# Kernel optimization log

Measured on AMD Instinct MI355X. Metric: run time of the kernel, lower is better.

## Reference

```python
import jax, jax.numpy as jnp
import numpy as np

EXPERT_NUM = 64
EXPERT_USE = 8
AUX_LOSS_LAMBDA = 0.01


def setup_inputs() -> dict:
    key = jax.random.key(0)
    k1, k2 = jax.random.split(key)
    h = jax.random.normal(k1, (4, 4096, 2048), dtype=jnp.float32)
    # nn.Linear(embed_dim, expert_num) weight: [expert_num, embed_dim], ~U(-1/sqrt(d), 1/sqrt(d))
    bound = 1.0 / np.sqrt(2048.0)
    W = jax.random.uniform(k2, (EXPERT_NUM, 2048), dtype=jnp.float32,
                           minval=-bound, maxval=bound)
    return {"h": h, "W": W}


def reference(h, W):
    b, s, d = h.shape
    hf = h.reshape(-1, d)                              # [b*s, d]
    logits = jnp.einsum('nd,ed->ne', hf, W)            # [b*s, E]
    scores = jax.nn.softmax(logits, axis=-1)           # [b*s, E]
    expert_scores, expert_ids = jax.lax.top_k(scores, EXPERT_USE)  # [b*s, k]
    expert_weight = expert_scores / jnp.sum(expert_scores, axis=-1, keepdims=True)
    # L2 load-balance aux loss (training mode, lambda > 0)
    seq_probs = scores.reshape(b, s, EXPERT_NUM).mean(axis=1)      # [b, E]
    aux_loss = jnp.mean(jnp.sum(seq_probs ** 2, axis=-1)) * EXPERT_NUM * AUX_LOSS_LAMBDA
    return expert_ids, expert_weight, aux_loss
```

## Files before the change

### kernel.cpp

```cpp
#include <hip/hip_runtime.h>
#include <math.h>

#define NTOK 16384
#define DIM 2048
#define NEXP 64
#define TOPK 8
#define BT 64
#define KC 32
#define NCHUNK (DIM / KC)
#define PADK 36
#define NBLK (NTOK / BT)
#define EPW 4

typedef float f2 __attribute__((ext_vector_type(2)));
typedef float f4 __attribute__((ext_vector_type(4)));

__device__ __forceinline__ f2 pk_mul(f2 a, f2 b) {
    f2 d; asm("v_pk_mul_f32 %0, %1, %2" : "=v"(d) : "v"(a), "v"(b)); return d;
}
__device__ __forceinline__ f2 pk_add(f2 a, f2 b) {
    f2 d; asm("v_pk_add_f32 %0, %1, %2" : "=v"(d) : "v"(a), "v"(b)); return d;
}

__global__ __launch_bounds__(1024, 1) void moe_gate_np(
    const float* __restrict__ h, const float* __restrict__ W,
    float* __restrict__ out, float* __restrict__ wsum)
{
#pragma clang fp contract(off)
    __shared__ float sA[2][BT * PADK];
    __shared__ float sB[2][NEXP * PADK];
    __shared__ float lg[BT][NEXP + 2];

    const int tid  = threadIdx.x;
    const int lane = tid & 63;
    const int wv   = tid >> 6;
    const int blk  = blockIdx.x;
    const long tok0 = (long)blk * BT;
    const float* hA = h + tok0 * DIM;
    const int e0 = wv * EPW;

    const int sidx = tid & 511;
    const int srow = sidx >> 3;
    const int scol = (sidx & 7) * 4;
    const bool isA = tid < 512;
    const float* gsrc = isA ? (hA + (long)srow * DIM + scol)
                            : (W  + (long)srow * DIM + scol);
    float* l0 = isA ? &sA[0][srow * PADK + scol] : &sB[0][srow * PADK + scol];
    float* l1 = isA ? &sA[1][srow * PADK + scol] : &sB[1][srow * PADK + scol];

    f4 pa = *(const f4*)gsrc;
    *(f4*)l0 = pa;
    pa = *(const f4*)(gsrc + KC);

    f2 a01[EPW], a23[EPW];
    #pragma unroll
    for (int j = 0; j < EPW; ++j) { a01[j] = (f2)(0.f); a23[j] = (f2)(0.f); }

    for (int kc = 0; kc < NCHUNK; ++kc) {
        __syncthreads();
        const int cur = kc & 1;

        if (kc + 1 < NCHUNK)
            *(f4*)(cur ? l0 : l1) = pa;
        if (kc + 2 < NCHUNK)
            pa = *(const f4*)(gsrc + (long)(kc + 2) * KC);

        #pragma unroll
        for (int s = 0; s < 2; ++s) {
            f4 af[4];
            const float* ab = &sA[cur][lane * PADK + s * 16];
            #pragma unroll
            for (int v = 0; v < 4; ++v) af[v] = *(const f4*)(ab + 4 * v);

            f2 alo[4], ahi[4];
            #pragma unroll
            for (int v = 0; v < 4; ++v) {
                alo[v] = __builtin_shufflevector(af[v], af[v], 0, 1);
                ahi[v] = __builtin_shufflevector(af[v], af[v], 2, 3);
            }

            const float* bb = &sB[cur][e0 * PADK + s * 16];
            #pragma unroll
            for (int j = 0; j < EPW; ++j) {
                f4 Bf[4];
                #pragma unroll
                for (int v = 0; v < 4; ++v)
                    Bf[v] = *(const f4*)(bb + j * PADK + 4 * v);

                f2 blo[4], bhi[4];
                #pragma unroll
                for (int v = 0; v < 4; ++v) {
                    blo[v] = __builtin_shufflevector(Bf[v], Bf[v], 0, 1);
                    bhi[v] = __builtin_shufflevector(Bf[v], Bf[v], 2, 3);
                }
                f2 x;
                x = pk_add(pk_mul(blo[3], alo[3]), a01[j]);
                x = pk_add(pk_mul(blo[2], alo[2]), x);
                x = pk_add(pk_mul(blo[1], alo[1]), x);
                a01[j] = pk_add(pk_mul(blo[0], alo[0]), x);
                x = pk_add(pk_mul(bhi[3], ahi[3]), a23[j]);
                x = pk_add(pk_mul(bhi[2], ahi[2]), x);
                x = pk_add(pk_mul(bhi[1], ahi[1]), x);
                a23[j] = pk_add(pk_mul(bhi[0], ahi[0]), x);
            }
        }
    }

    #pragma unroll
    for (int j = 0; j < EPW; ++j) {
        f2 s2 = pk_add(a01[j], a23[j]);
        lg[lane][e0 + j] = s2.x + s2.y;
    }
    __syncthreads();

    float auxacc = 0.f;

    for (int tt = 0; tt < 4; ++tt) {
        const int t = wv * 4 + tt;
        const float s = lg[t][lane];

        float m = s;
        #pragma unroll
        for (int off = 32; off >= 1; off >>= 1)
            m = fmaxf(m, __shfl_xor(m, off));

        const float p = expf(s - m);
        lg[t][lane] = p;
        __asm__ volatile("" ::: "memory");

        float r0s = lg[t][0], r1s = lg[t][1], r2s = lg[t][2], r3s = lg[t][3];
        float r4s = lg[t][4], r5s = lg[t][5], r6s = lg[t][6], r7s = lg[t][7];
        #pragma unroll
        for (int i = 1; i < 8; ++i) {
            r0s += lg[t][8 * i + 0]; r1s += lg[t][8 * i + 1];
            r2s += lg[t][8 * i + 2]; r3s += lg[t][8 * i + 3];
            r4s += lg[t][8 * i + 4]; r5s += lg[t][8 * i + 5];
            r6s += lg[t][8 * i + 6]; r7s += lg[t][8 * i + 7];
        }
        const float S = ((r0s + r1s) + (r2s + r3s)) + ((r4s + r5s) + (r6s + r7s));

        const float score = p / S;
        auxacc += score;

        float cv = score;
        float myv = 0.f;
        int   myi = 0;
        #pragma unroll
        for (int i = 0; i < TOPK; ++i) {
            float v = cv;
            int idx = lane;
            #pragma unroll
            for (int off = 32; off >= 1; off >>= 1) {
                float v2 = __shfl_xor(v, off);
                int   i2 = __shfl_xor(idx, off);
                if (v2 > v || (v2 == v && i2 < idx)) { v = v2; idx = i2; }
            }
            if (lane == i)   { myv = v; myi = idx; }
            if (lane == idx) cv = -1.f;
        }

        float S8 = 0.f;
        #pragma unroll
        for (int r = 0; r < TOPK; ++r) S8 += __shfl(myv, r);

        if (lane < TOPK) {
            const long o = (tok0 + t) * TOPK + lane;
            out[o]                     = (float)myi;
            out[(long)NTOK * TOPK + o] = myv / S8;
        }
    }

    const int b = blk >> 6;
    atomicAdd(&wsum[b * NEXP + lane], auxacc);
}

__global__ void aux_finish(const float* __restrict__ wsum, float* __restrict__ out)
{
    const int lane = threadIdx.x;
    float a = 0.f;
    #pragma unroll
    for (int b = 0; b < 4; ++b) {
        const float v = wsum[b * NEXP + lane] * (1.0f / 4096.0f);
        a = fmaf(v, v, a);
    }
    #pragma unroll
    for (int off = 32; off >= 1; off >>= 1)
        a += __shfl_xor(a, off);
    if (lane == 0)
        out[2L * NTOK * TOPK] = a * 0.25f * (float)NEXP * 0.01f;
}

extern "C" void kernel_launch(void* const* d_in, const int* in_sizes, int n_in,
                              void* d_out, int out_size, void* d_ws, size_t ws_size,
                              hipStream_t stream) {
    const float* h = (const float*)d_in[0];
    const float* W = (const float*)d_in[1];
    float* out  = (float*)d_out;
    float* wsum = (float*)d_ws;

    hipMemsetAsync(d_ws, 0, 1024, stream);
    moe_gate_np<<<NBLK, 1024, 0, stream>>>(h, W, out, wsum);
    aux_finish<<<1, 64, 0, stream>>>(wsum, out);
}
```

Measured before the change: 153.8 us.

## Load half of each wave's gate weights via scalar loads instead of LDS

```diff
diff --git a/kernel.cpp b/kernel.cpp
--- a/kernel.cpp
+++ b/kernel.cpp
@@ -12,9 +12,13 @@
 #define NBLK (NTOK / BT)
 #define EPW 4
 
-typedef float f2 __attribute__((ext_vector_type(2)));
-typedef float f4 __attribute__((ext_vector_type(4)));
-
+typedef float f2  __attribute__((ext_vector_type(2)));
+typedef float f4  __attribute__((ext_vector_type(4)));
+typedef float f16 __attribute__((ext_vector_type(16)));
+
+__device__ __forceinline__ f2 pk_mul_sv(f2 bs, f2 av) {
+    f2 d; asm("v_pk_mul_f32 %0, %1, %2" : "=v"(d) : "s"(bs), "v"(av)); return d;
+}
 __device__ __forceinline__ f2 pk_mul(f2 a, f2 b) {
     f2 d; asm("v_pk_mul_f32 %0, %1, %2" : "=v"(d) : "v"(a), "v"(b)); return d;
 }
@@ -28,7 +32,7 @@
 {
 #pragma clang fp contract(off)
     __shared__ float sA[2][BT * PADK];
-    __shared__ float sB[2][NEXP * PADK];
+    __shared__ float sBh[2][32 * PADK];
     __shared__ float lg[BT][NEXP + 2];
 
     const int tid  = threadIdx.x;
@@ -39,18 +43,27 @@
     const float* hA = h + tok0 * DIM;
     const int e0 = wv * EPW;
 
-    const int sidx = tid & 511;
-    const int srow = sidx >> 3;
-    const int scol = (sidx & 7) * 4;
-    const bool isA = tid < 512;
-    const float* gsrc = isA ? (hA + (long)srow * DIM + scol)
-                            : (W  + (long)srow * DIM + scol);
-    float* l0 = isA ? &sA[0][srow * PADK + scol] : &sB[0][srow * PADK + scol];
-    float* l1 = isA ? &sA[1][srow * PADK + scol] : &sB[1][srow * PADK + scol];
-
-    f4 pa = *(const f4*)gsrc;
-    *(f4*)l0 = pa;
-    pa = *(const f4*)(gsrc + KC);
+    const int e0s = __builtin_amdgcn_readfirstlane(wv) * EPW;
+    const float* wb = W + (long)e0s * DIM;
+
+    const bool isA  = tid < 512;
+    const bool doSt = tid < 768;
+    const int  aRow = (tid & 511) >> 3;
+    const int  aCol = (tid & 7) * 4;
+    const int  bRow = (tid - 512) >> 3;
+    const int  bExp = (bRow >> 1) * 4 + 2 + (bRow & 1);
+
+    const float* gsrc = isA ? (hA + (long)aRow * DIM + aCol)
+                            : (W  + (long)bExp * DIM + aCol);
+    float* l0 = isA ? &sA[0][aRow * PADK + aCol] : &sBh[0][bRow * PADK + aCol];
+    float* l1 = isA ? &sA[1][aRow * PADK + aCol] : &sBh[1][bRow * PADK + aCol];
+
+    f4 pa;
+    if (doSt) {
+        pa = *(const f4*)gsrc;
+        *(f4*)l0 = pa;
+        pa = *(const f4*)(gsrc + KC);
+    }
 
     f2 a01[EPW], a23[EPW];
     #pragma unroll
@@ -60,13 +73,27 @@
         __syncthreads();
         const int cur = kc & 1;
 
-        if (kc + 1 < NCHUNK)
+        if (doSt && kc + 1 < NCHUNK)
             *(f4*)(cur ? l0 : l1) = pa;
-        if (kc + 2 < NCHUNK)
+        if (doSt && kc + 2 < NCHUNK)
             pa = *(const f4*)(gsrc + (long)(kc + 2) * KC);
 
         #pragma unroll
         for (int s = 0; s < 2; ++s) {
+            const int kb = kc * KC + s * 16;
+
+            f16 Bs[2];
+            Bs[0] = *(const f16*)(wb + kb);
+            Bs[1] = *(const f16*)(wb + DIM + kb);
+
+            const float* bb = &sBh[cur][(2 * wv) * PADK + s * 16];
+            f4 Bl[2][4];
+            #pragma unroll
+            for (int v = 0; v < 4; ++v) {
+                Bl[0][v] = *(const f4*)(bb + 4 * v);
+                Bl[1][v] = *(const f4*)(bb + PADK + 4 * v);
+            }
+
             f4 af[4];
             const float* ab = &sA[cur][lane * PADK + s * 16];
             #pragma unroll
@@ -79,29 +106,45 @@
                 ahi[v] = __builtin_shufflevector(af[v], af[v], 2, 3);
             }
 
-            const float* bb = &sB[cur][e0 * PADK + s * 16];
-            #pragma unroll
-            for (int j = 0; j < EPW; ++j) {
-                f4 Bf[4];
-                #pragma unroll
-                for (int v = 0; v < 4; ++v)
-                    Bf[v] = *(const f4*)(bb + j * PADK + 4 * v);
-
+            #pragma unroll
+            for (int j = 0; j < 2; ++j) {
+                f2 blo[4], bhi[4];
+                blo[0] = __builtin_shufflevector(Bs[j], Bs[j],  0,  1);
+                bhi[0] = __builtin_shufflevector(Bs[j], Bs[j],  2,  3);
+                blo[1] = __builtin_shufflevector(Bs[j], Bs[j],  4,  5);
+                bhi[1] = __builtin_shufflevector(Bs[j], Bs[j],  6,  7);
+                blo[2] = __builtin_shufflevector(Bs[j], Bs[j],  8,  9);
+                bhi[2] = __builtin_shufflevector(Bs[j], Bs[j], 10, 11);
+                blo[3] = __builtin_shufflevector(Bs[j], Bs[j], 12, 13);
+                bhi[3] = __builtin_shufflevector(Bs[j], Bs[j], 14, 15);
+                f2 x;
+                x = pk_add(pk_mul_sv(blo[3], alo[3]), a01[j]);
+                x = pk_add(pk_mul_sv(blo[2], alo[2]), x);
+                x = pk_add(pk_mul_sv(blo[1], alo[1]), x);
+                a01[j] = pk_add(pk_mul_sv(blo[0], alo[0]), x);
+                x = pk_add(pk_mul_sv(bhi[3], ahi[3]), a23[j]);
+                x = pk_add(pk_mul_sv(bhi[2], ahi[2]), x);
+                x = pk_add(pk_mul_sv(bhi[1], ahi[1]), x);
+                a23[j] = pk_add(pk_mul_sv(bhi[0], ahi[0]), x);
+            }
+
+            #pragma unroll
+            for (int j = 0; j < 2; ++j) {
                 f2 blo[4], bhi[4];
                 #pragma unroll
                 for (int v = 0; v < 4; ++v) {
-                    blo[v] = __builtin_shufflevector(Bf[v], Bf[v], 0, 1);
-                    bhi[v] = __builtin_shufflevector(Bf[v], Bf[v], 2, 3);
+                    blo[v] = __builtin_shufflevector(Bl[j][v], Bl[j][v], 0, 1);
+                    bhi[v] = __builtin_shufflevector(Bl[j][v], Bl[j][v], 2, 3);
                 }
                 f2 x;
-                x = pk_add(pk_mul(blo[3], alo[3]), a01[j]);
+                x = pk_add(pk_mul(blo[3], alo[3]), a01[2 + j]);
                 x = pk_add(pk_mul(blo[2], alo[2]), x);
                 x = pk_add(pk_mul(blo[1], alo[1]), x);
-                a01[j] = pk_add(pk_mul(blo[0], alo[0]), x);
-                x = pk_add(pk_mul(bhi[3], ahi[3]), a23[j]);
+                a01[2 + j] = pk_add(pk_mul(blo[0], alo[0]), x);
+                x = pk_add(pk_mul(bhi[3], ahi[3]), a23[2 + j]);
                 x = pk_add(pk_mul(bhi[2], ahi[2]), x);
                 x = pk_add(pk_mul(bhi[1], ahi[1]), x);
-                a23[j] = pk_add(pk_mul(bhi[0], ahi[0]), x);
+                a23[2 + j] = pk_add(pk_mul(bhi[0], ahi[0]), x);
             }
         }
     }
```

After: 147.4 us. 1.04x faster.
